# Optimization experiments

Measured on AMD Instinct MI355X. Metric: run time of the kernel, lower is better.

## Reference

```python
import jax, jax.numpy as jnp
import numpy as np

VOCAB = 32000
D = 512        # input_dim == hid_dim
HID = 512
LAYERS = 2
B = 64
S = 2048
PAD = 0


def setup_inputs() -> dict:
    key = jax.random.key(0)
    ks = jax.random.split(key, 6)
    # indices in [1, VOCAB) so the padding row is never hit (PAD=0)
    src = jax.random.randint(ks[0], (B, S), 1, VOCAB, dtype=jnp.int64 if jax.config.read('jax_enable_x64') else jnp.int32)
    scale = 1.0 / np.sqrt(HID)
    embed = jax.random.normal(ks[1], (VOCAB, D), dtype=jnp.float32)
    embed = embed.at[PAD].set(0.0)  # padding_idx row is zero
    # nn.RNN weights: per layer W_ih [HID, in], W_hh [HID, HID], b_ih, b_hh [HID]
    W_ih = jax.random.uniform(ks[2], (LAYERS, HID, D), jnp.float32, -scale, scale)
    W_hh = jax.random.uniform(ks[3], (LAYERS, HID, HID), jnp.float32, -scale, scale)
    b_ih = jax.random.uniform(ks[4], (LAYERS, HID), jnp.float32, -scale, scale)
    b_hh = jax.random.uniform(ks[5], (LAYERS, HID), jnp.float32, -scale, scale)
    return {"src": src, "embed": embed, "W_ih": W_ih, "W_hh": W_hh,
            "b_ih": b_ih, "b_hh": b_hh}


def reference(src, embed, W_ih, W_hh, b_ih, b_hh):
    # src: [B, S] -> transpose to time-major [S, B], then embedding lookup
    x = embed[src.T]                      # [S, B, D]
    finals = []
    for l in range(LAYERS):
        wi, wh = W_ih[l], W_hh[l]
        bi, bh = b_ih[l], b_hh[l]
        xb = jnp.einsum('sbd,hd->sbh', x, wi) + bi + bh  # precompute input term
        def step(h, x_t):
            h_new = jnp.tanh(x_t + h @ wh.T)
            return h_new, h_new
        h0 = jnp.zeros((x.shape[1], HID), dtype=x.dtype)
        hT, ys = jax.lax.scan(step, h0, xb)
        finals.append(hT)
        x = ys                             # feed layer output to next layer
    # nn.RNN returns hidden of shape [n_layers, batch, hid_dim]
    return jnp.stack(finals, axis=0)
```

## Files before the change

kernel.cpp:

```cpp
#include <hip/hip_runtime.h>


#define SEQ 2048

typedef _Float16 half8 __attribute__((ext_vector_type(8)));
typedef float floatx4 __attribute__((ext_vector_type(4)));
typedef unsigned long long u64;

__device__ inline half8 cvt8(const float* p) {
    float4 f0 = ((const float4*)p)[0];
    float4 f1 = ((const float4*)p)[1];
    half8 h;
    h[0]=(_Float16)f0.x; h[1]=(_Float16)f0.y; h[2]=(_Float16)f0.z; h[3]=(_Float16)f0.w;
    h[4]=(_Float16)f1.x; h[5]=(_Float16)f1.y; h[6]=(_Float16)f1.z; h[7]=(_Float16)f1.w;
    return h;
}

__device__ inline u64 ld8(const void* p) {
    return __hip_atomic_load((const u64*)p, __ATOMIC_RELAXED, __HIP_MEMORY_SCOPE_AGENT);
}
__device__ inline half8 ldfrag(const _Float16* p) {
    union { u64 d[2]; half8 h; } u;
    u.d[0] = ld8(p);
    u.d[1] = ld8(p + 4);
    return u.h;
}

#define MFMA(a, b, c) __builtin_amdgcn_mfma_f32_16x16x32_f16((a), (b), (c), 0, 0, 0)

__global__ __launch_bounds__(256, 1)
void rnn_persist(const int* __restrict__ src, const float* __restrict__ embed,
                 const float* __restrict__ W_ih, const float* __restrict__ W_hh,
                 const float* __restrict__ b_ih, const float* __restrict__ b_hh,
                 float* __restrict__ out, _Float16* hbase, int* flags)
{
    const int tid = threadIdx.x;
    if (tid >= 64) return;

    const int lane = tid;
    const int g    = blockIdx.x;
    const int L    = g >> 7;
    const int bg   = (g >> 5) & 3;
    const int jg   = g & 31;
    const int q    = lane >> 4;
    const int rr   = lane & 15;
    const int col  = jg * 16 + rr;

    _Float16* h0s = hbase;
    _Float16* h1s = hbase + 4 * 64 * 512;

    half8 bw[32];
    {
        const float* Wi = W_ih + ((size_t)L * 512 + col) * 512;
        const float* Wh = W_hh + ((size_t)L * 512 + col) * 512;
        #pragma unroll
        for (int u = 0; u < 16; ++u) bw[u]      = cvt8(Wi + u * 32 + q * 8);
        #pragma unroll
        for (int u = 0; u < 16; ++u) bw[16 + u] = cvt8(Wh + u * 32 + q * 8);
    }
    const float bias = b_ih[L * 512 + col] + b_hh[L * 512 + col];

    const int arow = bg * 16 + rr;
    int* flg = flags + bg * 64;
    const int lf = lane >> 5;

    for (int t = 0; t < SEQ; ++t) {
        floatx4 acc0 = {0.f,0.f,0.f,0.f}, acc1 = {0.f,0.f,0.f,0.f};

        if (L == 0) {
            const int erow = src[arow * SEQ + t];
            const float* eb = embed + (size_t)erow * 512 + q * 8;
            half8 ax[16];
            #pragma unroll
            for (int u = 0; u < 16; ++u) ax[u] = cvt8(eb + u * 32);
            #pragma unroll
            for (int u = 0; u < 16; ++u) {
                if (u & 1) acc1 = MFMA(ax[u], bw[u], acc1);
                else       acc0 = MFMA(ax[u], bw[u], acc0);
            }
            const int tgt = (lf == 0) ? t : (t - 3);
            for (long it = 0; it < (1L << 26); ++it) {
                int v = __hip_atomic_load(&flg[lane], __ATOMIC_RELAXED,
                                          __HIP_MEMORY_SCOPE_AGENT);
                if (__ballot(v >= tgt) == ~0ull) break;
                __builtin_amdgcn_s_sleep(1);
            }
            __atomic_signal_fence(__ATOMIC_SEQ_CST);
            if (t > 0) {
                const _Float16* hb = h0s + ((t - 1) & 3) * (64 * 512)
                                   + arow * 512 + q * 8;
                half8 ah[16];
                #pragma unroll
                for (int u = 0; u < 16; ++u) ah[u] = ldfrag(hb + u * 32);
                #pragma unroll
                for (int u = 0; u < 16; ++u) {
                    if (u & 1) acc1 = MFMA(ah[u], bw[16 + u], acc1);
                    else       acc0 = MFMA(ah[u], bw[16 + u], acc0);
                }
            }
        } else {
            const int tgt = (lf == 0) ? (t + 1) : t;
            for (long it = 0; it < (1L << 26); ++it) {
                int v = __hip_atomic_load(&flg[lane], __ATOMIC_RELAXED,
                                          __HIP_MEMORY_SCOPE_AGENT);
                if (__ballot(v >= tgt) == ~0ull) break;
                __builtin_amdgcn_s_sleep(1);
            }
            __atomic_signal_fence(__ATOMIC_SEQ_CST);
            {
                const _Float16* xa = h0s + (t & 3) * (64 * 512)
                                   + arow * 512 + q * 8;
                half8 ax[16];
                #pragma unroll
                for (int u = 0; u < 16; ++u) ax[u] = ldfrag(xa + u * 32);
                #pragma unroll
                for (int u = 0; u < 16; ++u) {
                    if (u & 1) acc1 = MFMA(ax[u], bw[u], acc1);
                    else       acc0 = MFMA(ax[u], bw[u], acc0);
                }
            }
            if (t > 0) {
                const _Float16* hb = h1s + ((t - 1) & 3) * (64 * 512)
                                   + arow * 512 + q * 8;
                half8 ah[16];
                #pragma unroll
                for (int u = 0; u < 16; ++u) ah[u] = ldfrag(hb + u * 32);
                #pragma unroll
                for (int u = 0; u < 16; ++u) {
                    if (u & 1) acc1 = MFMA(ah[u], bw[16 + u], acc1);
                    else       acc0 = MFMA(ah[u], bw[16 + u], acc0);
                }
            }
        }

        float hv[4];
        #pragma unroll
        for (int r = 0; r < 4; ++r)
            hv[r] = tanhf(acc0[r] + acc1[r] + bias);

        if (t == SEQ - 1) {
            #pragma unroll
            for (int r = 0; r < 4; ++r)
                out[(size_t)L * 64 * 512 + (size_t)(bg * 16 + q * 4 + r) * 512 + col]
                    = hv[r];
        }

        {
            _Float16* hw = ((L == 0) ? h0s : h1s) + (t & 3) * (64 * 512)
                         + (size_t)(bg * 16) * 512 + col;
            #pragma unroll
            for (int r = 0; r < 4; ++r) {
                union { _Float16 f; unsigned short u; } cv;
                cv.f = (_Float16)hv[r];
                __hip_atomic_store((unsigned short*)(hw + (q * 4 + r) * 512),
                                   cv.u, __ATOMIC_RELAXED,
                                   __HIP_MEMORY_SCOPE_AGENT);
            }
        }
        __atomic_signal_fence(__ATOMIC_SEQ_CST);
        __builtin_amdgcn_s_waitcnt(0);
        __atomic_signal_fence(__ATOMIC_SEQ_CST);
        if (lane == 0)
            __hip_atomic_store(&flg[L * 32 + jg], t + 1, __ATOMIC_RELAXED,
                               __HIP_MEMORY_SCOPE_AGENT);
    }
}

extern "C" void kernel_launch(void* const* d_in, const int* in_sizes, int n_in,
                              void* d_out, int out_size, void* d_ws, size_t ws_size,
                              hipStream_t stream) {
    const int*   src   = (const int*)  d_in[0];
    const float* embed = (const float*)d_in[1];
    const float* W_ih  = (const float*)d_in[2];
    const float* W_hh  = (const float*)d_in[3];
    const float* b_ih  = (const float*)d_in[4];
    const float* b_hh  = (const float*)d_in[5];
    float*     out   = (float*)d_out;
    int*       flags = (int*)d_ws;
    _Float16*  hbase = (_Float16*)((char*)d_ws + 16384);

    hipMemsetAsync(d_ws, 0, 16384, stream);

    rnn_persist<<<dim3(256), dim3(256), 0, stream>>>(
        src, embed, W_ih, W_hh, b_ih, b_hh, out, hbase, flags);
}
```

Before: 15.18 ms.

## Use workgroup-scope L2 atomics for cross-block handoff with runtime probe fallback

Restructures the persistent RNN so each block holds both layers as two wavefronts. Only half the launched blocks do work, with the block index laid out so each batch group's blocks may share an XCD. It then runs a short probe in which the hidden-state exchange is written through both agent-scope and workgroup-scope (L2-local) atomics and compared. If the fast path is coherent, the remaining steps use the cheaper workgroup-scope atomic RMW loads and stores to avoid L3/MALL round trips. Otherwise it sleeps and falls back to agent-scope. This relies on block-to-XCD placement, which is not guaranteed and risks incorrect results if the probe passes by chance.

```diff
diff --git a/kernel.cpp b/kernel.cpp
--- a/kernel.cpp
+++ b/kernel.cpp
@@ -1,7 +1,8 @@
 #include <hip/hip_runtime.h>
 
 
-#define SEQ 2048
+#define SEQ   2048
+#define PROBE 8
 
 typedef _Float16 half8 __attribute__((ext_vector_type(8)));
 typedef float floatx4 __attribute__((ext_vector_type(4)));
@@ -16,39 +17,327 @@
     return h;
 }
 
-__device__ inline u64 ld8(const void* p) {
+__device__ inline u64 ld8_l3(const void* p) {
     return __hip_atomic_load((const u64*)p, __ATOMIC_RELAXED, __HIP_MEMORY_SCOPE_AGENT);
 }
-__device__ inline half8 ldfrag(const _Float16* p) {
+__device__ inline half8 ldfrag_l3(const _Float16* p) {
     union { u64 d[2]; half8 h; } u;
-    u.d[0] = ld8(p);
-    u.d[1] = ld8(p + 4);
+    u.d[0] = ld8_l3(p); u.d[1] = ld8_l3(p + 4);
     return u.h;
 }
+__device__ inline int ldflag_l3(const int* p) {
+    return __hip_atomic_load(p, __ATOMIC_RELAXED, __HIP_MEMORY_SCOPE_AGENT);
+}
+__device__ inline void st2_l3(_Float16* p, unsigned short v) {
+    __hip_atomic_store((unsigned short*)p, v, __ATOMIC_RELAXED, __HIP_MEMORY_SCOPE_AGENT);
+}
+__device__ inline void stflag_l3(int* p, int v) {
+    __hip_atomic_store(p, v, __ATOMIC_RELAXED, __HIP_MEMORY_SCOPE_AGENT);
+}
+
+__device__ inline u64 rmw8(_Float16* p) {
+    return __hip_atomic_fetch_add((u64*)(void*)p, 0ull, __ATOMIC_RELAXED,
+                                  __HIP_MEMORY_SCOPE_WORKGROUP);
+}
+__device__ inline half8 ldfrag_l2(_Float16* p) {
+    union { u64 d[2]; half8 h; } u;
+    u.d[0] = rmw8(p); u.d[1] = rmw8(p + 4);
+    return u.h;
+}
+__device__ inline int ldflag_l2(int* p) {
+    return __hip_atomic_fetch_add(p, 0, __ATOMIC_RELAXED,
+                                  __HIP_MEMORY_SCOPE_WORKGROUP);
+}
+__device__ inline void st2_l2(_Float16* p, unsigned short v) {
+    __hip_atomic_store((unsigned short*)p, v, __ATOMIC_RELAXED,
+                       __HIP_MEMORY_SCOPE_WORKGROUP);
+}
+__device__ inline void stflag_l2(int* p, int v) {
+    __hip_atomic_store(p, v, __ATOMIC_RELAXED, __HIP_MEMORY_SCOPE_WORKGROUP);
+}
+
+__device__ inline int neq8(half8 a, half8 b) {
+    union { half8 h; u64 d[2]; } ua, ub; ua.h = a; ub.h = b;
+    return (ua.d[0] != ub.d[0]) | (ua.d[1] != ub.d[1]);
+}
 
 #define MFMA(a, b, c) __builtin_amdgcn_mfma_f32_16x16x32_f16((a), (b), (c), 0, 0, 0)
 
-__global__ __launch_bounds__(256, 1)
+template<int M>
+__device__ __forceinline__ void run_range(
+    const int t0, const int lane, const int L, const int bg, const int jg,
+    const int* __restrict__ src, const float* __restrict__ embed,
+    const half8* bw, const float bias, float* __restrict__ out,
+    _Float16* h0s, _Float16* h1s, int* flg)
+{
+    const int q    = lane >> 4;
+    const int rr   = lane & 15;
+    const int col  = jg * 16 + rr;
+    const int arow = bg * 16 + rr;
+    const int lf   = lane >> 5;
+    int degraded = 0;
+
+    for (int t = t0; t < SEQ; ++t) {
+        floatx4 acc0 = {0.f,0.f,0.f,0.f}, acc1 = {0.f,0.f,0.f,0.f};
+
+        if (L == 0) {
+            const int erow = src[arow * SEQ + t];
+            const float* eb = embed + (size_t)erow * 512 + q * 8;
+            half8 ax[16];
+            #pragma unroll
+            for (int u = 0; u < 16; ++u) ax[u] = cvt8(eb + u * 32);
+            #pragma unroll
+            for (int u = 0; u < 16; ++u) {
+                if (u & 1) acc1 = MFMA(ax[u], bw[u], acc1);
+                else       acc0 = MFMA(ax[u], bw[u], acc0);
+            }
+            const int tgt = (lf == 0) ? t : (t - 3);
+            {
+                const long bound = (M == 0) ? (1L << 26)
+                                            : (degraded ? 64 : (1L << 16));
+                bool ok = false;
+                for (long it = 0; it < bound; ++it) {
+                    int v = (M == 0) ? ldflag_l3(&flg[lane]) : ldflag_l2(&flg[lane]);
+                    if (__ballot(v >= tgt) == ~0ull) { ok = true; break; }
+                    __builtin_amdgcn_s_sleep(1);
+                }
+                if (!ok) degraded = 1;
+            }
+            __atomic_signal_fence(__ATOMIC_SEQ_CST);
+            if (t > 0) {
+                _Float16* hb = h0s + ((t - 1) & 3) * (64 * 512) + arow * 512 + q * 8;
+                half8 ah[16];
+                #pragma unroll
+                for (int u = 0; u < 16; ++u)
+                    ah[u] = (M == 0) ? ldfrag_l3(hb + u * 32) : ldfrag_l2(hb + u * 32);
+                #pragma unroll
+                for (int u = 0; u < 16; ++u) {
+                    if (u & 1) acc1 = MFMA(ah[u], bw[16 + u], acc1);
+                    else       acc0 = MFMA(ah[u], bw[16 + u], acc0);
+                }
+            }
+        } else {
+            const int tgt = (lf == 0) ? (t + 1) : t;
+            {
+                const long bound = (M == 0) ? (1L << 26)
+                                            : (degraded ? 64 : (1L << 16));
+                bool ok = false;
+                for (long it = 0; it < bound; ++it) {
+                    int v = (M == 0) ? ldflag_l3(&flg[lane]) : ldflag_l2(&flg[lane]);
+                    if (__ballot(v >= tgt) == ~0ull) { ok = true; break; }
+                    __builtin_amdgcn_s_sleep(1);
+                }
+                if (!ok) degraded = 1;
+            }
+            __atomic_signal_fence(__ATOMIC_SEQ_CST);
+            {
+                _Float16* xa = h0s + (t & 3) * (64 * 512) + arow * 512 + q * 8;
+                half8 ax[16];
+                #pragma unroll
+                for (int u = 0; u < 16; ++u)
+                    ax[u] = (M == 0) ? ldfrag_l3(xa + u * 32) : ldfrag_l2(xa + u * 32);
+                #pragma unroll
+                for (int u = 0; u < 16; ++u) {
+                    if (u & 1) acc1 = MFMA(ax[u], bw[u], acc1);
+                    else       acc0 = MFMA(ax[u], bw[u], acc0);
+                }
+            }
+            if (t > 0) {
+                _Float16* hb = h1s + ((t - 1) & 3) * (64 * 512) + arow * 512 + q * 8;
+                half8 ah[16];
+                #pragma unroll
+                for (int u = 0; u < 16; ++u)
+                    ah[u] = (M == 0) ? ldfrag_l3(hb + u * 32) : ldfrag_l2(hb + u * 32);
+                #pragma unroll
+                for (int u = 0; u < 16; ++u) {
+                    if (u & 1) acc1 = MFMA(ah[u], bw[16 + u], acc1);
+                    else       acc0 = MFMA(ah[u], bw[16 + u], acc0);
+                }
+            }
+        }
+
+        float hv[4];
+        #pragma unroll
+        for (int r = 0; r < 4; ++r)
+            hv[r] = tanhf(acc0[r] + acc1[r] + bias);
+
+        if (t == SEQ - 1) {
+            #pragma unroll
+            for (int r = 0; r < 4; ++r)
+                out[(size_t)L * 64 * 512 + (size_t)(bg * 16 + q * 4 + r) * 512 + col]
+                    = hv[r];
+        }
+
+        {
+            _Float16* hw = ((L == 0) ? h0s : h1s) + (t & 3) * (64 * 512)
+                         + (size_t)(bg * 16) * 512 + col;
+            #pragma unroll
+            for (int r = 0; r < 4; ++r) {
+                union { _Float16 f; unsigned short u; } cv;
+                cv.f = (_Float16)hv[r];
+                if (M == 0) st2_l3(hw + (q * 4 + r) * 512, cv.u);
+                else        st2_l2(hw + (q * 4 + r) * 512, cv.u);
+            }
+        }
+        __atomic_signal_fence(__ATOMIC_SEQ_CST);
+        __builtin_amdgcn_s_waitcnt(0);
+        __atomic_signal_fence(__ATOMIC_SEQ_CST);
+        if (lane == 0) {
+            if (M == 0) stflag_l3(&flg[L * 32 + jg], t + 1);
+            else        stflag_l2(&flg[L * 32 + jg], t + 1);
+        }
+    }
+}
+
+__device__ __forceinline__ void run_probe(
+    const int lane, const int L, const int bg, const int jg,
+    const int* __restrict__ src, const float* __restrict__ embed,
+    const half8* bw, const float bias,
+    _Float16* h0s, _Float16* h1s, int* flg,
+    _Float16* f0s, _Float16* f1s, int* flgF,
+    int* verdict)
+{
+    const int q    = lane >> 4;
+    const int rr   = lane & 15;
+    const int col  = jg * 16 + rr;
+    const int arow = bg * 16 + rr;
+    const int lf   = lane >> 5;
+    int bad = 0;
+
+    for (int t = 0; t < PROBE; ++t) {
+        floatx4 acc0 = {0.f,0.f,0.f,0.f}, acc1 = {0.f,0.f,0.f,0.f};
+        const int tgt = (L == 0) ? ((lf == 0) ? t : (t - 3))
+                                 : ((lf == 0) ? (t + 1) : t);
+
+        if (L == 0) {
+            const int erow = src[arow * SEQ + t];
+            const float* eb = embed + (size_t)erow * 512 + q * 8;
+            half8 ax[16];
+            #pragma unroll
+            for (int u = 0; u < 16; ++u) ax[u] = cvt8(eb + u * 32);
+            #pragma unroll
+            for (int u = 0; u < 16; ++u) {
+                if (u & 1) acc1 = MFMA(ax[u], bw[u], acc1);
+                else       acc0 = MFMA(ax[u], bw[u], acc0);
+            }
+        }
+
+        for (long it = 0; it < (1L << 26); ++it) {
+            int v = ldflag_l3(&flg[lane]);
+            if (__ballot(v >= tgt) == ~0ull) break;
+            __builtin_amdgcn_s_sleep(1);
+        }
+        __atomic_signal_fence(__ATOMIC_SEQ_CST);
+
+        {
+            bool ok = false;
+            for (long it = 0; it < 256; ++it) {
+                int v = ldflag_l2(&flgF[lane]);
+                if (__ballot(v >= tgt) == ~0ull) { ok = true; break; }
+                __builtin_amdgcn_s_sleep(1);
+            }
+            if (!ok) bad = 1;
+        }
+
+        if (L == 0) {
+            if (t > 0) {
+                const size_t off = ((t - 1) & 3) * (64 * 512) + arow * 512 + q * 8;
+                half8 ah[16];
+                #pragma unroll
+                for (int u = 0; u < 16; ++u) {
+                    ah[u] = ldfrag_l3(h0s + off + u * 32);
+                    half8 fh = ldfrag_l2(f0s + off + u * 32);
+                    bad |= neq8(ah[u], fh);
+                }
+                #pragma unroll
+                for (int u = 0; u < 16; ++u) {
+                    if (u & 1) acc1 = MFMA(ah[u], bw[16 + u], acc1);
+                    else       acc0 = MFMA(ah[u], bw[16 + u], acc0);
+                }
+            }
+        } else {
+            {
+                const size_t off = (t & 3) * (64 * 512) + arow * 512 + q * 8;
+                half8 ax[16];
+                #pragma unroll
+                for (int u = 0; u < 16; ++u) {
+                    ax[u] = ldfrag_l3(h0s + off + u * 32);
+                    half8 fh = ldfrag_l2(f0s + off + u * 32);
+                    bad |= neq8(ax[u], fh);
+                }
+                #pragma unroll
+                for (int u = 0; u < 16; ++u) {
+                    if (u & 1) acc1 = MFMA(ax[u], bw[u], acc1);
+                    else       acc0 = MFMA(ax[u], bw[u], acc0);
+                }
+            }
+            if (t > 0) {
+                const size_t off = ((t - 1) & 3) * (64 * 512) + arow * 512 + q * 8;
+                half8 ah[16];
+                #pragma unroll
+                for (int u = 0; u < 16; ++u) {
+                    ah[u] = ldfrag_l3(h1s + off + u * 32);
+                    half8 fh = ldfrag_l2(f1s + off + u * 32);
+                    bad |= neq8(ah[u], fh);
+                }
+                #pragma unroll
+                for (int u = 0; u < 16; ++u) {
+                    if (u & 1) acc1 = MFMA(ah[u], bw[16 + u], acc1);
+                    else       acc0 = MFMA(ah[u], bw[16 + u], acc0);
+                }
+            }
+        }
+
+        float hv[4];
+        #pragma unroll
+        for (int r = 0; r < 4; ++r)
+            hv[r] = tanhf(acc0[r] + acc1[r] + bias);
+
+        {
+            const size_t off = (t & 3) * (64 * 512) + (size_t)(bg * 16) * 512 + col;
+            _Float16* hwS = ((L == 0) ? h0s : h1s) + off;
+            _Float16* hwF = ((L == 0) ? f0s : f1s) + off;
+            #pragma unroll
+            for (int r = 0; r < 4; ++r) {
+                union { _Float16 f; unsigned short u; } cv;
+                cv.f = (_Float16)hv[r];
+                st2_l3(hwS + (q * 4 + r) * 512, cv.u);
+                st2_l2(hwF + (q * 4 + r) * 512, cv.u);
+            }
+        }
+        if (t == PROBE - 1) {
+            const int anybad = (__ballot(bad) != 0ull) ? 1 : 0;
+            if (lane == 0 && anybad)
+                __hip_atomic_fetch_or(verdict, 1, __ATOMIC_RELAXED,
+                                      __HIP_MEMORY_SCOPE_AGENT);
+        }
+        __atomic_signal_fence(__ATOMIC_SEQ_CST);
+        __builtin_amdgcn_s_waitcnt(0);
+        __atomic_signal_fence(__ATOMIC_SEQ_CST);
+        if (lane == 0) {
+            stflag_l2(&flgF[L * 32 + jg], t + 1);
+            stflag_l3(&flg[L * 32 + jg], t + 1);
+        }
+    }
+}
+
+__global__ __launch_bounds__(128, 1)
 void rnn_persist(const int* __restrict__ src, const float* __restrict__ embed,
                  const float* __restrict__ W_ih, const float* __restrict__ W_hh,
                  const float* __restrict__ b_ih, const float* __restrict__ b_hh,
-                 float* __restrict__ out, _Float16* hbase, int* flags)
+                 float* __restrict__ out, _Float16* hS, _Float16* hF,
+                 int* flagsS, int* flagsF, int* verdict)
 {
+    const int b = blockIdx.x;
+    if ((b & 7) >= 4) return;
+    const int bg  = b & 7;
+    const int jg  = b >> 3;
     const int tid = threadIdx.x;
-    if (tid >= 64) return;
-
-    const int lane = tid;
-    const int g    = blockIdx.x;
-    const int L    = g >> 7;
-    const int bg   = (g >> 5) & 3;
-    const int jg   = g & 31;
-    const int q    = lane >> 4;
-    const int rr   = lane & 15;
-    const int col  = jg * 16 + rr;
-
-    _Float16* h0s = hbase;
-    _Float16* h1s = hbase + 4 * 64 * 512;
-
+    const int lane = tid & 63;
+    const int L    = tid >> 6;
+
+    const int q = lane >> 4, rr = lane & 15;
+    const int col = jg * 16 + rr;
     half8 bw[32];
     {
         const float* Wi = W_ih + ((size_t)L * 512 + col) * 512;
@@ -60,109 +349,30 @@
     }
     const float bias = b_ih[L * 512 + col] + b_hh[L * 512 + col];
 
-    const int arow = bg * 16 + rr;
-    int* flg = flags + bg * 64;
-    const int lf = lane >> 5;
-
-    for (int t = 0; t < SEQ; ++t) {
-        floatx4 acc0 = {0.f,0.f,0.f,0.f}, acc1 = {0.f,0.f,0.f,0.f};
-
-        if (L == 0) {
-            const int erow = src[arow * SEQ + t];
-            const float* eb = embed + (size_t)erow * 512 + q * 8;
-            half8 ax[16];
-            #pragma unroll
-            for (int u = 0; u < 16; ++u) ax[u] = cvt8(eb + u * 32);
-            #pragma unroll
-            for (int u = 0; u < 16; ++u) {
-                if (u & 1) acc1 = MFMA(ax[u], bw[u], acc1);
-                else       acc0 = MFMA(ax[u], bw[u], acc0);
-            }
-            const int tgt = (lf == 0) ? t : (t - 3);
-            for (long it = 0; it < (1L << 26); ++it) {
-                int v = __hip_atomic_load(&flg[lane], __ATOMIC_RELAXED,
-                                          __HIP_MEMORY_SCOPE_AGENT);
-                if (__ballot(v >= tgt) == ~0ull) break;
-                __builtin_amdgcn_s_sleep(1);
-            }
-            __atomic_signal_fence(__ATOMIC_SEQ_CST);
-            if (t > 0) {
-                const _Float16* hb = h0s + ((t - 1) & 3) * (64 * 512)
-                                   + arow * 512 + q * 8;
-                half8 ah[16];
-                #pragma unroll
-                for (int u = 0; u < 16; ++u) ah[u] = ldfrag(hb + u * 32);
-                #pragma unroll
-                for (int u = 0; u < 16; ++u) {
-                    if (u & 1) acc1 = MFMA(ah[u], bw[16 + u], acc1);
-                    else       acc0 = MFMA(ah[u], bw[16 + u], acc0);
-                }
-            }
-        } else {
-            const int tgt = (lf == 0) ? (t + 1) : t;
-            for (long it = 0; it < (1L << 26); ++it) {
-                int v = __hip_atomic_load(&flg[lane], __ATOMIC_RELAXED,
-                                          __HIP_MEMORY_SCOPE_AGENT);
-                if (__ballot(v >= tgt) == ~0ull) break;
-                __builtin_amdgcn_s_sleep(1);
-            }
-            __atomic_signal_fence(__ATOMIC_SEQ_CST);
-            {
-                const _Float16* xa = h0s + (t & 3) * (64 * 512)
-                                   + arow * 512 + q * 8;
-                half8 ax[16];
-                #pragma unroll
-                for (int u = 0; u < 16; ++u) ax[u] = ldfrag(xa + u * 32);
-                #pragma unroll
-                for (int u = 0; u < 16; ++u) {
-                    if (u & 1) acc1 = MFMA(ax[u], bw[u], acc1);
-                    else       acc0 = MFMA(ax[u], bw[u], acc0);
-                }
-            }
-            if (t > 0) {
-                const _Float16* hb = h1s + ((t - 1) & 3) * (64 * 512)
-                                   + arow * 512 + q * 8;
-                half8 ah[16];
-                #pragma unroll
-                for (int u = 0; u < 16; ++u) ah[u] = ldfrag(hb + u * 32);
-                #pragma unroll
-                for (int u = 0; u < 16; ++u) {
-                    if (u & 1) acc1 = MFMA(ah[u], bw[16 + u], acc1);
-                    else       acc0 = MFMA(ah[u], bw[16 + u], acc0);
-                }
-            }
-        }
-
-        float hv[4];
-        #pragma unroll
-        for (int r = 0; r < 4; ++r)
-            hv[r] = tanhf(acc0[r] + acc1[r] + bias);
-
-        if (t == SEQ - 1) {
-            #pragma unroll
-            for (int r = 0; r < 4; ++r)
-                out[(size_t)L * 64 * 512 + (size_t)(bg * 16 + q * 4 + r) * 512 + col]
-                    = hv[r];
-        }
-
-        {
-            _Float16* hw = ((L == 0) ? h0s : h1s) + (t & 3) * (64 * 512)
-                         + (size_t)(bg * 16) * 512 + col;
-            #pragma unroll
-            for (int r = 0; r < 4; ++r) {
-                union { _Float16 f; unsigned short u; } cv;
-                cv.f = (_Float16)hv[r];
-                __hip_atomic_store((unsigned short*)(hw + (q * 4 + r) * 512),
-                                   cv.u, __ATOMIC_RELAXED,
-                                   __HIP_MEMORY_SCOPE_AGENT);
-            }
-        }
-        __atomic_signal_fence(__ATOMIC_SEQ_CST);
-        __builtin_amdgcn_s_waitcnt(0);
-        __atomic_signal_fence(__ATOMIC_SEQ_CST);
-        if (lane == 0)
-            __hip_atomic_store(&flg[L * 32 + jg], t + 1, __ATOMIC_RELAXED,
-                               __HIP_MEMORY_SCOPE_AGENT);
+    _Float16* h0sS = hS;  _Float16* h1sS = hS + 4 * 64 * 512;
+    _Float16* h0sF = hF;  _Float16* h1sF = hF + 4 * 64 * 512;
+    int* flgS = flagsS + bg * 64;
+    int* flgF = flagsF + bg * 64;
+
+    run_probe(lane, L, bg, jg, src, embed, bw, bias,
+              h0sS, h1sS, flgS, h0sF, h1sF, flgF, &verdict[bg]);
+
+    for (long it = 0; it < (1L << 26); ++it) {
+        int v = ldflag_l3(&flgS[lane]);
+        if (__ballot(v >= PROBE) == ~0ull) break;
+        __builtin_amdgcn_s_sleep(1);
+    }
+    __atomic_signal_fence(__ATOMIC_SEQ_CST);
+    const int vd = __hip_atomic_load(&verdict[bg], __ATOMIC_RELAXED,
+                                     __HIP_MEMORY_SCOPE_AGENT);
+
+    if (vd == 0) {
+        run_range<1>(PROBE, lane, L, bg, jg, src, embed, bw, bias, out,
+                     h0sF, h1sF, flgF);
+    } else {
+        for (int i = 0; i < 600; ++i) __builtin_amdgcn_s_sleep(125);
+        run_range<0>(PROBE, lane, L, bg, jg, src, embed, bw, bias, out,
+                     h0sS, h1sS, flgS);
     }
 }
 
@@ -175,12 +385,16 @@
     const float* W_hh  = (const float*)d_in[3];
     const float* b_ih  = (const float*)d_in[4];
     const float* b_hh  = (const float*)d_in[5];
-    float*     out   = (float*)d_out;
-    int*       flags = (int*)d_ws;
-    _Float16*  hbase = (_Float16*)((char*)d_ws + 16384);
+    float* out = (float*)d_out;
+
+    int*      flagsS  = (int*)d_ws;
+    int*      flagsF  = (int*)d_ws + 256;
+    int*      verdict = (int*)d_ws + 512;
+    _Float16* hS = (_Float16*)((char*)d_ws + 16384);
+    _Float16* hF = hS + 8 * 64 * 512;
 
     hipMemsetAsync(d_ws, 0, 16384, stream);
 
-    rnn_persist<<<dim3(256), dim3(256), 0, stream>>>(
-        src, embed, W_ih, W_hh, b_ih, b_hh, out, hbase, flags);
-}
+    rnn_persist<<<dim3(256), dim3(128), 0, stream>>>(
+        src, embed, W_ih, W_hh, b_ih, b_hh, out, hS, hF, flagsS, flagsF, verdict);
+}
```

Result: slower. 29.03 ms (+91.3%).

## Prefetch next-step embeddings via LDS and coalesce hidden-state stores

Applied to the files above, without the earlier changes.

Layer-0 blocks now fetch the next timestep's embedding row into a double-buffered LDS area using global_load_lds, so the embedding load overlaps the current step's spin-wait and recurrent MFMA work instead of sitting on the critical path. Hidden-state outputs are staged through LDS and written as 8-byte atomic stores rather than scattered 2-byte stores. The block size also shrinks to one wavefront. The trade-off is extra LDS round trips and waitcnt barriers on every step, and the staging buffer is reused, which adds a possible hazard with in-flight prefetches.

```diff
diff --git a/kernel.cpp b/kernel.cpp
--- a/kernel.cpp
+++ b/kernel.cpp
@@ -26,18 +26,23 @@
     return u.h;
 }
 
+__device__ inline void glds16(const float* g, const float* l) {
+    __builtin_amdgcn_global_load_lds(
+        (const __attribute__((address_space(1))) void*)g,
+        (__attribute__((address_space(3))) void*)l, 16, 0, 0);
+}
+
 #define MFMA(a, b, c) __builtin_amdgcn_mfma_f32_16x16x32_f16((a), (b), (c), 0, 0, 0)
 
-__global__ __launch_bounds__(256, 1)
+__global__ __launch_bounds__(64, 1)
 void rnn_persist(const int* __restrict__ src, const float* __restrict__ embed,
                  const float* __restrict__ W_ih, const float* __restrict__ W_hh,
                  const float* __restrict__ b_ih, const float* __restrict__ b_hh,
                  float* __restrict__ out, _Float16* hbase, int* flags)
 {
-    const int tid = threadIdx.x;
-    if (tid >= 64) return;
-
-    const int lane = tid;
+    __shared__ float ebuf[2][16][2][64][4];
+
+    const int lane = threadIdx.x;
     const int g    = blockIdx.x;
     const int L    = g >> 7;
     const int bg   = (g >> 5) & 3;
@@ -64,19 +69,41 @@
     int* flg = flags + bg * 64;
     const int lf = lane >> 5;
 
+    if (L == 0) {
+        const int e0 = src[arow * SEQ];
+        const float* eb = embed + (size_t)e0 * 512 + q * 8;
+        #pragma unroll
+        for (int u = 0; u < 16; ++u) {
+            glds16(eb + u * 32,     &ebuf[0][u][0][0][0]);
+            glds16(eb + u * 32 + 4, &ebuf[0][u][1][0][0]);
+        }
+    }
+
     for (int t = 0; t < SEQ; ++t) {
         floatx4 acc0 = {0.f,0.f,0.f,0.f}, acc1 = {0.f,0.f,0.f,0.f};
+        const int cur = t & 1;
 
         if (L == 0) {
-            const int erow = src[arow * SEQ + t];
-            const float* eb = embed + (size_t)erow * 512 + q * 8;
-            half8 ax[16];
-            #pragma unroll
-            for (int u = 0; u < 16; ++u) ax[u] = cvt8(eb + u * 32);
+            asm volatile("s_waitcnt vmcnt(0)" ::: "memory");
+            __builtin_amdgcn_sched_barrier(0);
             #pragma unroll
             for (int u = 0; u < 16; ++u) {
-                if (u & 1) acc1 = MFMA(ax[u], bw[u], acc1);
-                else       acc0 = MFMA(ax[u], bw[u], acc0);
+                float4 f0 = *reinterpret_cast<const float4*>(&ebuf[cur][u][0][lane][0]);
+                float4 f1 = *reinterpret_cast<const float4*>(&ebuf[cur][u][1][lane][0]);
+                half8 a;
+                a[0]=(_Float16)f0.x; a[1]=(_Float16)f0.y; a[2]=(_Float16)f0.z; a[3]=(_Float16)f0.w;
+                a[4]=(_Float16)f1.x; a[5]=(_Float16)f1.y; a[6]=(_Float16)f1.z; a[7]=(_Float16)f1.w;
+                if (u & 1) acc1 = MFMA(a, bw[u], acc1);
+                else       acc0 = MFMA(a, bw[u], acc0);
+            }
+            if (t + 1 < SEQ) {
+                const int en = src[arow * SEQ + t + 1];
+                const float* eb = embed + (size_t)en * 512 + q * 8;
+                #pragma unroll
+                for (int u = 0; u < 16; ++u) {
+                    glds16(eb + u * 32,     &ebuf[cur ^ 1][u][0][0][0]);
+                    glds16(eb + u * 32 + 4, &ebuf[cur ^ 1][u][1][0][0]);
+                }
             }
             const int tgt = (lf == 0) ? t : (t - 3);
             for (long it = 0; it < (1L << 26); ++it) {
@@ -146,16 +173,18 @@
         }
 
         {
-            _Float16* hw = ((L == 0) ? h0s : h1s) + (t & 3) * (64 * 512)
-                         + (size_t)(bg * 16) * 512 + col;
+            _Float16* hb2 = (_Float16*)&ebuf[(L == 0) ? cur : 0][0][0][0][0];
             #pragma unroll
-            for (int r = 0; r < 4; ++r) {
-                union { _Float16 f; unsigned short u; } cv;
-                cv.f = (_Float16)hv[r];
-                __hip_atomic_store((unsigned short*)(hw + (q * 4 + r) * 512),
-                                   cv.u, __ATOMIC_RELAXED,
-                                   __HIP_MEMORY_SCOPE_AGENT);
-            }
+            for (int r = 0; r < 4; ++r)
+                hb2[(q * 4 + r) * 16 + rr] = (_Float16)hv[r];
+            asm volatile("s_waitcnt lgkmcnt(0)" ::: "memory");
+            __builtin_amdgcn_sched_barrier(0);
+            const int lrow = lane >> 2, seg = lane & 3;
+            u64 v = *reinterpret_cast<const u64*>(&hb2[lrow * 16 + seg * 4]);
+            _Float16* dst = ((L == 0) ? h0s : h1s) + (t & 3) * (64 * 512)
+                          + (size_t)(bg * 16 + lrow) * 512 + jg * 16 + seg * 4;
+            __hip_atomic_store((u64*)dst, v, __ATOMIC_RELAXED,
+                               __HIP_MEMORY_SCOPE_AGENT);
         }
         __atomic_signal_fence(__ATOMIC_SEQ_CST);
         __builtin_amdgcn_s_waitcnt(0);
@@ -181,6 +210,6 @@
 
     hipMemsetAsync(d_ws, 0, 16384, stream);
 
-    rnn_persist<<<dim3(256), dim3(256), 0, stream>>>(
+    rnn_persist<<<dim3(256), dim3(64), 0, stream>>>(
         src, embed, W_ih, W_hh, b_ih, b_hh, out, hbase, flags);
 }
```

Measured after the change: 18.81 ms. 23.9% more time.
